# Performance work log

Hardware: AMD Instinct MI355X
Metric: run time of the kernel (lower is better)

Reference implementation:

```python
import jax, jax.numpy as jnp
import numpy as np

N_EMBD = 2048
N_HEAD = 16
N_KV_HEAD = 4
HEAD_DIM = N_EMBD // N_HEAD
MAX_SEQ_LEN = 2048
EPS = 1e-6
ROPE_THETA = 10000.0


def _build_rope_cache(dim, max_seq_len, theta=ROPE_THETA):
    inv_freq = 1.0 / theta ** (np.arange(0, dim, 2, dtype=np.float32) / dim)
    t = np.arange(max_seq_len, dtype=np.float32)
    freqs = np.outer(t, inv_freq)
    emb = np.concatenate([freqs, freqs], axis=-1)
    return jnp.asarray(np.cos(emb)), jnp.asarray(np.sin(emb))


def _rotate_half(x):
    x1, x2 = jnp.split(x, 2, axis=-1)
    return jnp.concatenate([-x2, x1], axis=-1)


def _rms_norm(x, w, eps=EPS):
    var = jnp.mean(jnp.square(x), axis=-1, keepdims=True)
    return x * jax.lax.rsqrt(var + eps) * w


def setup_inputs() -> dict:
    key = jax.random.key(0)
    ks = jax.random.split(key, 7)
    s = 1.0 / np.sqrt(N_EMBD)
    kv_dim = N_KV_HEAD * HEAD_DIM
    x = jax.random.normal(ks[0], (2, 2048, N_EMBD), dtype=jnp.float32)
    Wq = jax.random.normal(ks[1], (N_EMBD, N_EMBD), dtype=jnp.float32) * s
    Wk = jax.random.normal(ks[2], (kv_dim, N_EMBD), dtype=jnp.float32) * s
    Wv = jax.random.normal(ks[3], (kv_dim, N_EMBD), dtype=jnp.float32) * s
    Wo = jax.random.normal(ks[4], (N_EMBD, N_EMBD), dtype=jnp.float32) * s
    qn_w = jnp.ones((HEAD_DIM,), dtype=jnp.float32)
    kn_w = jnp.ones((HEAD_DIM,), dtype=jnp.float32)
    cos, sin = _build_rope_cache(HEAD_DIM, MAX_SEQ_LEN)
    return {"x": x, "Wq": Wq, "Wk": Wk, "Wv": Wv, "Wo": Wo,
            "qn_w": qn_w, "kn_w": kn_w, "rope_cos": cos, "rope_sin": sin}


def reference(x, Wq, Wk, Wv, Wo, qn_w, kn_w, rope_cos, rope_sin):
    B, T, C = x.shape
    # projections (torch Linear: y = x @ W.T)
    q = jnp.einsum('btc,dc->btd', x, Wq).reshape(B, T, N_HEAD, HEAD_DIM).transpose(0, 2, 1, 3)
    k = jnp.einsum('btc,dc->btd', x, Wk).reshape(B, T, N_KV_HEAD, HEAD_DIM).transpose(0, 2, 1, 3)
    v = jnp.einsum('btc,dc->btd', x, Wv).reshape(B, T, N_KV_HEAD, HEAD_DIM).transpose(0, 2, 1, 3)
    # qk rms-norm
    q = _rms_norm(q, qn_w)
    k = _rms_norm(k, kn_w)
    # rope
    cos = rope_cos[:T][None, None]  # [1,1,T,D]
    sin = rope_sin[:T][None, None]
    q = q * cos + _rotate_half(q) * sin
    k = k * cos + _rotate_half(k) * sin
    # GQA broadcast: group queries over kv heads instead of repeating k/v
    G = N_HEAD // N_KV_HEAD
    qg = q.reshape(B, N_KV_HEAD, G, T, HEAD_DIM)
    scale = 1.0 / jnp.sqrt(jnp.asarray(HEAD_DIM, dtype=q.dtype))
    scores = jnp.einsum('bhgqd,bhkd->bhgqk', qg, k) * scale  # [B,KV,G,T,T]
    causal = jnp.tril(jnp.ones((T, T), dtype=bool))
    scores = jnp.where(causal, scores, jnp.asarray(-jnp.inf, dtype=scores.dtype))
    attn = jax.nn.softmax(scores, axis=-1)
    y = jnp.einsum('bhgqk,bhkd->bhgqd', attn, v)  # [B,KV,G,T,D]
    y = y.reshape(B, N_HEAD, T, HEAD_DIM).transpose(0, 2, 1, 3).reshape(B, T, C)
    return jnp.einsum('btc,dc->btd', y, Wo)
```

## Files before the change

### kernel.cpp

```cpp
#include <hip/hip_runtime.h>
#include <stdint.h>

typedef unsigned short u16;
typedef __attribute__((ext_vector_type(4))) float f32x4;
typedef __attribute__((ext_vector_type(16))) float f32x16;
typedef __attribute__((ext_vector_type(8))) short bf16x8;
typedef __attribute__((ext_vector_type(4))) unsigned short u16x4;
typedef __attribute__((ext_vector_type(4))) unsigned u32x4;

static __device__ __forceinline__ u16 f2bf(float f) {
  union { float f; unsigned u; } v; v.f = f;
  unsigned r = v.u + 0x7fffu + ((v.u >> 16) & 1u);
  return (u16)(r >> 16);
}

static __device__ __forceinline__ unsigned cvtpk(float lo, float hi) {
  unsigned r;
  asm("v_cvt_pk_bf16_f32 %0, %1, %2" : "=v"(r) : "v"(lo), "v"(hi));
  return r;
}

static __device__ __forceinline__ void plane32_swap(unsigned& a, unsigned& b) {
  asm volatile("v_permlane32_swap_b32 %0, %1" : "+v"(a), "+v"(b));
}

static __device__ __forceinline__ void load_lds16(const void* g, void* l) {
  __builtin_amdgcn_global_load_lds(
      (const __attribute__((address_space(1))) void*)g,
      (__attribute__((address_space(3))) void*)l, 16, 0, 0);
}


__global__ __launch_bounds__(256) void cvt_f32_bf16(
    const float* __restrict__ in, u16* __restrict__ out, int n) {
  int i = blockIdx.x * 256 + threadIdx.x;
  const int n4 = n >> 2;
  for (; i < n4; i += gridDim.x * 256) {
    f32x4 v = *(const f32x4*)(in + (size_t)i * 4);
    u16x4 o = { f2bf(v[0]), f2bf(v[1]), f2bf(v[2]), f2bf(v[3]) };
    *(u16x4*)(out + (size_t)i * 4) = o;
  }
}

__global__ __launch_bounds__(256) void build_wcat(
    const float* __restrict__ Wq, const float* __restrict__ Wk,
    const float* __restrict__ Wv, u16* __restrict__ out) {
  int i = blockIdx.x * 256 + threadIdx.x;
  const int n4 = 3072 * 512;
  for (; i < n4; i += gridDim.x * 256) {
    int row = i >> 9;
    int c4 = i & 511;
    const float* src;
    if (row < 2048)       src = Wq + (size_t)row * 2048;
    else if (row < 2560)  src = Wk + (size_t)(row - 2048) * 2048;
    else                  src = Wv + (size_t)(row - 2560) * 2048;
    f32x4 v = *(const f32x4*)(src + c4 * 4);
    u16x4 o = { f2bf(v[0]), f2bf(v[1]), f2bf(v[2]), f2bf(v[3]) };
    *(u16x4*)(out + (size_t)i * 4) = o;
  }
}

__global__ __launch_bounds__(256) void gemm_bt(
    const u16* __restrict__ A, const u16* __restrict__ B,
    float* __restrict__ C, int M, int N, int K) {
  __shared__ u16 As[128 * 32];
  __shared__ u16 Bs[128 * 32];
  const int tid = threadIdx.x;
  const int lin = blockIdx.x;
  const int x = lin & 7, t = lin >> 3;
  const int bm = x * 4 + (t & 3);
  const int bn = t >> 2;
  const int w = tid >> 6, l = tid & 63;
  const int wr = w >> 1, wc = w & 1;
  const int lr = l & 15, lg = l >> 4;
  f32x4 acc[4][4] = {};
  const int srow = tid >> 2;
  const int scol = (tid & 3) << 3;
  const u16* Ag = A + (size_t)bm * 128 * K + (size_t)srow * K + scol;
  const u16* Bg = B + (size_t)bn * 128 * K + (size_t)srow * K + scol;
  u16* Asl = As + srow * 32 + scol;
  u16* Bsl = Bs + srow * 32 + scol;
  const int nk = K >> 5;
  for (int kt = 0; kt < nk; ++kt) {
    __syncthreads();
    const int ko = kt << 5;
    load_lds16(Ag + ko, Asl);
    load_lds16(Ag + (size_t)64 * K + ko, Asl + 64 * 32);
    load_lds16(Bg + ko, Bsl);
    load_lds16(Bg + (size_t)64 * K + ko, Bsl + 64 * 32);
    __syncthreads();
    bf16x8 af[4], bfr[4];
#pragma unroll
    for (int m = 0; m < 4; ++m)
      af[m] = *(const bf16x8*)&As[(wr * 64 + m * 16 + lr) * 32 + lg * 8];
#pragma unroll
    for (int n = 0; n < 4; ++n)
      bfr[n] = *(const bf16x8*)&Bs[(wc * 64 + n * 16 + lr) * 32 + lg * 8];
#pragma unroll
    for (int m = 0; m < 4; ++m)
#pragma unroll
      for (int n = 0; n < 4; ++n)
        acc[m][n] = __builtin_amdgcn_mfma_f32_16x16x32_bf16(af[m], bfr[n], acc[m][n], 0, 0, 0);
  }
#pragma unroll
  for (int m = 0; m < 4; ++m) {
    const int row = bm * 128 + wr * 64 + m * 16 + lg * 4;
#pragma unroll
    for (int n = 0; n < 4; ++n) {
      const int col = bn * 128 + wc * 64 + n * 16 + lr;
#pragma unroll
      for (int r = 0; r < 4; ++r)
        C[(size_t)(row + r) * N + col] = acc[m][n][r];
    }
  }
}

__global__ __launch_bounds__(256) void norm_rope(
    const float* __restrict__ qkv, const float* __restrict__ qn_w,
    const float* __restrict__ kn_w, const float* __restrict__ cosb,
    const float* __restrict__ sinb, u16* __restrict__ qhat,
    u16* __restrict__ khat) {
  const int gw = (blockIdx.x * 256 + threadIdx.x) >> 6;
  const int lane = threadIdx.x & 63;
  const int slot = gw % 20;
  const int row = gw / 20;
  const int t = row & 2047;
  const int b = row >> 11;
  const float* src; const float* nw; u16* dst;
  bool isq = slot < 16;
  if (isq) {
    src = qkv + (size_t)row * 3072 + slot * 128;
    nw = qn_w;
    dst = qhat + ((size_t)(b * 16 + slot) * 2048 + t) * 128;
  } else {
    src = qkv + (size_t)row * 3072 + 2048 + (slot - 16) * 128;
    nw = kn_w;
    dst = khat + ((size_t)(b * 4 + (slot - 16)) * 2048 + t) * 128;
  }
  float x1 = src[lane], x2 = src[lane + 64];
  float ss = x1 * x1 + x2 * x2;
#pragma unroll
  for (int o = 32; o; o >>= 1) ss += __shfl_xor(ss, o);
  float rs = rsqrtf(ss * (1.0f / 128.0f) + 1e-6f);
  float h1 = x1 * rs * nw[lane];
  float h2 = x2 * rs * nw[lane + 64];
  float c = cosb[t * 128 + lane], s = sinb[t * 128 + lane];
  float o1 = h1 * c - h2 * s;
  float o2 = h2 * c + h1 * s;
  if (isq) { o1 *= 0.088388347648318447f; o2 *= 0.088388347648318447f; }
  dst[lane] = f2bf(o1);
  dst[lane + 64] = f2bf(o2);
}

__global__ __launch_bounds__(256) void v_trans(
    const float* __restrict__ qkv, u16* __restrict__ vT) {
  __shared__ u16 st[64][130];
  const int bi = blockIdx.x;
  const int tt = bi & 31;
  const int kv = (bi >> 5) & 3;
  const int b = bi >> 7;
  const int tid = threadIdx.x;
#pragma unroll
  for (int i = 0; i < 32; ++i) {
    int idx = i * 256 + tid;
    int t = idx >> 7, d = idx & 127;
    float v = qkv[(size_t)(b * 2048 + tt * 64 + t) * 3072 + 2560 + kv * 128 + d];
    st[t][d] = f2bf(v);
  }
  __syncthreads();
#pragma unroll
  for (int i = 0; i < 32; ++i) {
    int idx = i * 256 + tid;
    int d = idx >> 6, t = idx & 63;
    vT[((size_t)(b * 4 + kv) * 128 + d) * 2048 + tt * 64 + t] = st[t][d];
  }
}

__global__ __launch_bounds__(512, 2) void attn(
    const u16* __restrict__ qhat, const u16* __restrict__ khat,
    const u16* __restrict__ vT, u16* __restrict__ yb) {
  __shared__ u16 Kt[2][64 * 128];
  const int bi = blockIdx.x;
  const int s = bi & 7;
  const int bh = bi >> 3;
  const int h = bh & 15, b = bh >> 4;
  const int kvh = h >> 2;
  const int tid = threadIdx.x;
  const int w = tid >> 6, l = tid & 63;
  const int ws = w & 3;
  const int cw = (w < 4) ? s : (15 - s);
  const int ql = l & 31, hi = l >> 5;
  const int wq0 = cw * 128 + ws * 32;
  const int wq_end = wq0 + 31;
  const int qg = wq0 + ql;

  bf16x8 qf[8];
  const u16* qp = qhat + ((size_t)(b * 16 + h) * 2048 + qg) * 128 + hi * 8;
#pragma unroll
  for (int sf = 0; sf < 8; ++sf) qf[sf] = *(const bf16x8*)(qp + 16 * sf);

  f32x16 yacc[4] = {};
  float m = -1e30f, lsum = 0.f;

  const u16* Kg = khat + (size_t)(b * 4 + kvh) * 2048 * 128;
  const u16* Vg = vT + (size_t)(b * 4 + kvh) * 128 * 2048;
  const int nt = 32 - 2 * s;

  auto stageK = [&](int tile, int buf) {
#pragma unroll
    for (int j = 0; j < 2; ++j) {
      int idx = j * 512 + tid;
      int row = idx >> 4, ch = idx & 15;
      load_lds16(Kg + (size_t)(tile * 64 + row) * 128 + ((ch ^ (row & 7)) * 8),
                 &Kt[buf][idx * 8]);
    }
  };

  stageK(0, 0);
  int cur = 0;
  for (int tile = 0; tile < nt; ++tile) {
    const int kv0 = tile * 64;
    __syncthreads();
    if (tile + 1 < nt) stageK(tile + 1, cur ^ 1);
    if (kv0 <= wq_end) {
      const u16* Vrow = Vg + (size_t)ql * 2048 + kv0 + hi * 8;
      bf16x8 va[4], vb[4];
#pragma unroll
      for (int ks = 0; ks < 4; ++ks) va[ks] = *(const bf16x8*)(Vrow + ks * 16);
#pragma unroll
      for (int ks = 0; ks < 4; ++ks) vb[ks] = *(const bf16x8*)(Vrow + 32 * 2048 + ks * 16);
      const u16* Kc = Kt[cur];
      f32x16 sacc[2] = {};
      __builtin_amdgcn_s_setprio(1);
#pragma unroll
      for (int n = 0; n < 2; ++n) {
#pragma unroll
        for (int sf = 0; sf < 8; ++sf) {
          bf16x8 kf = *(const bf16x8*)&Kc[(n * 32 + ql) * 128 + (((2 * sf + hi) ^ (l & 7)) * 8)];
          sacc[n] = __builtin_amdgcn_mfma_f32_32x32x16_bf16(kf, qf[sf], sacc[n], 0, 0, 0);
        }
      }
      __builtin_amdgcn_s_setprio(0);
      if (kv0 + 63 > wq0) {
#pragma unroll
        for (int n = 0; n < 2; ++n)
#pragma unroll
          for (int r = 0; r < 16; ++r) {
            int kv = kv0 + n * 32 + (r & 3) + 8 * (r >> 2) + 4 * hi;
            if (kv > qg) sacc[n][r] = -1e30f;
          }
      }
      float pm = -1e30f;
#pragma unroll
      for (int n = 0; n < 2; ++n)
#pragma unroll
        for (int r = 0; r < 16; ++r) pm = fmaxf(pm, sacc[n][r]);
      pm = fmaxf(pm, __shfl_xor(pm, 32));
      if (!__all(pm - m <= 8.0f)) {
        float mn = fmaxf(m, pm);
        float sc = __expf(m - mn);
        m = mn;
        lsum *= sc;
#pragma unroll
        for (int r = 0; r < 16; ++r) {
          int row = (r & 3) + 8 * (r >> 2) + 4 * hi;
          float scr = __shfl(sc, row);
#pragma unroll
          for (int d = 0; d < 4; ++d) yacc[d][r] *= scr;
        }
      }
      float ls = 0.f;
#pragma unroll
      for (int n = 0; n < 2; ++n)
#pragma unroll
        for (int r = 0; r < 16; ++r) {
          float e = __expf(sacc[n][r] - m);
          sacc[n][r] = e;
          ls += e;
        }
      ls += __shfl_xor(ls, 32);
      lsum += ls;
      bf16x8 pa[4];
#pragma unroll
      for (int s4 = 0; s4 < 4; ++s4) {
        const int n = s4 >> 1, R = (s4 & 1) * 8;
        unsigned P01 = cvtpk(sacc[n][R + 0], sacc[n][R + 1]);
        unsigned P23 = cvtpk(sacc[n][R + 2], sacc[n][R + 3]);
        unsigned P45 = cvtpk(sacc[n][R + 4], sacc[n][R + 5]);
        unsigned P67 = cvtpk(sacc[n][R + 6], sacc[n][R + 7]);
        plane32_swap(P01, P45);
        plane32_swap(P23, P67);
        union { u32x4 u; bf16x8 bv; } cvu;
        cvu.u[0] = P01; cvu.u[1] = P23; cvu.u[2] = P45; cvu.u[3] = P67;
        pa[s4] = cvu.bv;
      }
      __builtin_amdgcn_s_setprio(1);
#pragma unroll
      for (int ks = 0; ks < 4; ++ks)
        yacc[0] = __builtin_amdgcn_mfma_f32_32x32x16_bf16(pa[ks], va[ks], yacc[0], 0, 0, 0);
#pragma unroll
      for (int ks = 0; ks < 4; ++ks) va[ks] = *(const bf16x8*)(Vrow + 64 * 2048 + ks * 16);
#pragma unroll
      for (int ks = 0; ks < 4; ++ks)
        yacc[1] = __builtin_amdgcn_mfma_f32_32x32x16_bf16(pa[ks], vb[ks], yacc[1], 0, 0, 0);
#pragma unroll
      for (int ks = 0; ks < 4; ++ks) vb[ks] = *(const bf16x8*)(Vrow + 96 * 2048 + ks * 16);
#pragma unroll
      for (int ks = 0; ks < 4; ++ks)
        yacc[2] = __builtin_amdgcn_mfma_f32_32x32x16_bf16(pa[ks], va[ks], yacc[2], 0, 0, 0);
#pragma unroll
      for (int ks = 0; ks < 4; ++ks)
        yacc[3] = __builtin_amdgcn_mfma_f32_32x32x16_bf16(pa[ks], vb[ks], yacc[3], 0, 0, 0);
      __builtin_amdgcn_s_setprio(0);
    }
    cur ^= 1;
  }
#pragma unroll
  for (int r = 0; r < 16; ++r) {
    int row = (r & 3) + 8 * (r >> 2) + 4 * hi;
    float li = __shfl(lsum, row);
    float inv = 1.0f / li;
    u16* yp = yb + ((size_t)(b * 2048) + wq0 + row) * 2048 + h * 128 + ql;
#pragma unroll
    for (int d = 0; d < 4; ++d) yp[d * 32] = f2bf(yacc[d][r] * inv);
  }
}


extern "C" void kernel_launch(void* const* d_in, const int* in_sizes, int n_in,
                              void* d_out, int out_size, void* d_ws, size_t ws_size,
                              hipStream_t stream) {
  const float* x    = (const float*)d_in[0];
  const float* Wq   = (const float*)d_in[1];
  const float* Wk   = (const float*)d_in[2];
  const float* Wv   = (const float*)d_in[3];
  const float* Wo   = (const float*)d_in[4];
  const float* qn   = (const float*)d_in[5];
  const float* kn   = (const float*)d_in[6];
  const float* cosb = (const float*)d_in[7];
  const float* sinb = (const float*)d_in[8];
  float* out = (float*)d_out;
  (void)in_sizes; (void)n_in; (void)out_size; (void)ws_size;

  char* p = (char*)d_ws;
  u16*   xb   = (u16*)p;   p += (size_t)8388608 * 2;
  u16*   wcat = (u16*)p;   p += (size_t)6291456 * 2;
  u16*   wob  = (u16*)p;   p += (size_t)4194304 * 2;
  float* qkvf = (float*)p; p += (size_t)12582912 * 4;
  u16*   qh   = (u16*)p;   p += (size_t)8388608 * 2;
  u16*   kh   = (u16*)p;   p += (size_t)2097152 * 2;
  u16*   vt   = (u16*)p;   p += (size_t)2097152 * 2;
  u16*   yb   = (u16*)p;   p += (size_t)8388608 * 2;

  cvt_f32_bf16<<<2048, 256, 0, stream>>>(x, xb, 8388608);
  build_wcat<<<2048, 256, 0, stream>>>(Wq, Wk, Wv, wcat);
  cvt_f32_bf16<<<2048, 256, 0, stream>>>(Wo, wob, 4194304);
  gemm_bt<<<768, 256, 0, stream>>>(xb, wcat, qkvf, 4096, 3072, 2048);
  norm_rope<<<20480, 256, 0, stream>>>(qkvf, qn, kn, cosb, sinb, qh, kh);
  v_trans<<<256, 256, 0, stream>>>(qkvf, vt);
  attn<<<256, 512, 0, stream>>>(qh, kh, vt, yb);
  gemm_bt<<<512, 256, 0, stream>>>(yb, wob, out, 4096, 2048, 2048);
}
```

Baseline: 261.1 us.

## Split attention KV tiles across two wave groups and merge partial softmax results

The attention kernel doubles to 1024 threads: each 64-key tile is split so two groups of eight waves each handle 32 keys for the same query rows. At the end the partial max, sum and output accumulators are merged through shared memory before the normalized result is written. Separately, the softmax switches from __expf to a raw v_exp_f32 (exp2), with log2(e) folded into the query scale and the rescale threshold adjusted to match. The aim is more parallel work per block and cheaper exponentials, at the cost of extra LDS, merge synchronisation and register pressure from launch_bounds(1024,4).

Result: slower. 377.1 us (+44.4%).

```diff
diff --git a/kernel.cpp b/kernel.cpp
--- a/kernel.cpp
+++ b/kernel.cpp
@@ -22,6 +22,12 @@
 
 static __device__ __forceinline__ void plane32_swap(unsigned& a, unsigned& b) {
   asm volatile("v_permlane32_swap_b32 %0, %1" : "+v"(a), "+v"(b));
+}
+
+static __device__ __forceinline__ float exp2_fast(float x) {
+  float r;
+  asm("v_exp_f32 %0, %1" : "=v"(r) : "v"(x));
+  return r;
 }
 
 static __device__ __forceinline__ void load_lds16(const void* g, void* l) {
@@ -147,7 +153,7 @@
   float c = cosb[t * 128 + lane], s = sinb[t * 128 + lane];
   float o1 = h1 * c - h2 * s;
   float o2 = h2 * c + h1 * s;
-  if (isq) { o1 *= 0.088388347648318447f; o2 *= 0.088388347648318447f; }
+  if (isq) { o1 *= 0.12751744752f; o2 *= 0.12751744752f; }
   dst[lane] = f2bf(o1);
   dst[lane + 64] = f2bf(o2);
 }
@@ -176,10 +182,12 @@
   }
 }
 
-__global__ __launch_bounds__(512, 2) void attn(
+__global__ __launch_bounds__(1024, 4) void attn(
     const u16* __restrict__ qhat, const u16* __restrict__ khat,
     const u16* __restrict__ vT, u16* __restrict__ yb) {
   __shared__ u16 Kt[2][64 * 128];
+  __shared__ float obuf[4][32][128];
+  __shared__ float mlbuf[16][2][32];
   const int bi = blockIdx.x;
   const int s = bi & 7;
   const int bh = bi >> 3;
@@ -188,7 +196,9 @@
   const int tid = threadIdx.x;
   const int w = tid >> 6, l = tid & 63;
   const int ws = w & 3;
-  const int cw = (w < 4) ? s : (15 - s);
+  const int role = (w >> 2) & 1;
+  const int g = w >> 3;
+  const int cw = role ? (15 - s) : s;
   const int ql = l & 31, hi = l >> 5;
   const int wq0 = cw * 128 + ws * 32;
   const int wq_end = wq0 + 31;
@@ -206,59 +216,48 @@
   const u16* Vg = vT + (size_t)(b * 4 + kvh) * 128 * 2048;
   const int nt = 32 - 2 * s;
 
+  const int srow = tid >> 4, sch = tid & 15;
   auto stageK = [&](int tile, int buf) {
-#pragma unroll
-    for (int j = 0; j < 2; ++j) {
-      int idx = j * 512 + tid;
-      int row = idx >> 4, ch = idx & 15;
-      load_lds16(Kg + (size_t)(tile * 64 + row) * 128 + ((ch ^ (row & 7)) * 8),
-                 &Kt[buf][idx * 8]);
-    }
+    load_lds16(Kg + (size_t)(tile * 64 + srow) * 128 + ((sch ^ (srow & 7)) * 8),
+               &Kt[buf][tid * 8]);
   };
 
   stageK(0, 0);
   int cur = 0;
   for (int tile = 0; tile < nt; ++tile) {
-    const int kv0 = tile * 64;
+    const int kvb = tile * 64 + g * 32;
     __syncthreads();
     if (tile + 1 < nt) stageK(tile + 1, cur ^ 1);
-    if (kv0 <= wq_end) {
-      const u16* Vrow = Vg + (size_t)ql * 2048 + kv0 + hi * 8;
-      bf16x8 va[4], vb[4];
-#pragma unroll
-      for (int ks = 0; ks < 4; ++ks) va[ks] = *(const bf16x8*)(Vrow + ks * 16);
-#pragma unroll
-      for (int ks = 0; ks < 4; ++ks) vb[ks] = *(const bf16x8*)(Vrow + 32 * 2048 + ks * 16);
+    if (kvb <= wq_end) {
+      const u16* Vrow = Vg + (size_t)ql * 2048 + kvb + hi * 8;
+      bf16x8 va[2], vb[2];
+#pragma unroll
+      for (int ks = 0; ks < 2; ++ks) va[ks] = *(const bf16x8*)(Vrow + ks * 16);
+#pragma unroll
+      for (int ks = 0; ks < 2; ++ks) vb[ks] = *(const bf16x8*)(Vrow + 32 * 2048 + ks * 16);
       const u16* Kc = Kt[cur];
-      f32x16 sacc[2] = {};
+      f32x16 sacc = {};
       __builtin_amdgcn_s_setprio(1);
 #pragma unroll
-      for (int n = 0; n < 2; ++n) {
-#pragma unroll
-        for (int sf = 0; sf < 8; ++sf) {
-          bf16x8 kf = *(const bf16x8*)&Kc[(n * 32 + ql) * 128 + (((2 * sf + hi) ^ (l & 7)) * 8)];
-          sacc[n] = __builtin_amdgcn_mfma_f32_32x32x16_bf16(kf, qf[sf], sacc[n], 0, 0, 0);
+      for (int sf = 0; sf < 8; ++sf) {
+        bf16x8 kf = *(const bf16x8*)&Kc[(g * 32 + ql) * 128 + (((2 * sf + hi) ^ (l & 7)) * 8)];
+        sacc = __builtin_amdgcn_mfma_f32_32x32x16_bf16(kf, qf[sf], sacc, 0, 0, 0);
+      }
+      __builtin_amdgcn_s_setprio(0);
+      if (kvb + 31 > wq0) {
+#pragma unroll
+        for (int r = 0; r < 16; ++r) {
+          int kv = kvb + (r & 3) + 8 * (r >> 2) + 4 * hi;
+          if (kv > qg) sacc[r] = -1e30f;
         }
       }
-      __builtin_amdgcn_s_setprio(0);
-      if (kv0 + 63 > wq0) {
-#pragma unroll
-        for (int n = 0; n < 2; ++n)
-#pragma unroll
-          for (int r = 0; r < 16; ++r) {
-            int kv = kv0 + n * 32 + (r & 3) + 8 * (r >> 2) + 4 * hi;
-            if (kv > qg) sacc[n][r] = -1e30f;
-          }
-      }
       float pm = -1e30f;
 #pragma unroll
-      for (int n = 0; n < 2; ++n)
-#pragma unroll
-        for (int r = 0; r < 16; ++r) pm = fmaxf(pm, sacc[n][r]);
+      for (int r = 0; r < 16; ++r) pm = fmaxf(pm, sacc[r]);
       pm = fmaxf(pm, __shfl_xor(pm, 32));
-      if (!__all(pm - m <= 8.0f)) {
+      if (!__all(pm - m <= 11.0f)) {
         float mn = fmaxf(m, pm);
-        float sc = __expf(m - mn);
+        float sc = exp2_fast(m - mn);
         m = mn;
         lsum *= sc;
 #pragma unroll
@@ -271,58 +270,95 @@
       }
       float ls = 0.f;
 #pragma unroll
-      for (int n = 0; n < 2; ++n)
-#pragma unroll
-        for (int r = 0; r < 16; ++r) {
-          float e = __expf(sacc[n][r] - m);
-          sacc[n][r] = e;
-          ls += e;
-        }
+      for (int r = 0; r < 16; ++r) {
+        float e = exp2_fast(sacc[r] - m);
+        sacc[r] = e;
+        ls += e;
+      }
       ls += __shfl_xor(ls, 32);
       lsum += ls;
-      bf16x8 pa[4];
-#pragma unroll
-      for (int s4 = 0; s4 < 4; ++s4) {
-        const int n = s4 >> 1, R = (s4 & 1) * 8;
-        unsigned P01 = cvtpk(sacc[n][R + 0], sacc[n][R + 1]);
-        unsigned P23 = cvtpk(sacc[n][R + 2], sacc[n][R + 3]);
-        unsigned P45 = cvtpk(sacc[n][R + 4], sacc[n][R + 5]);
-        unsigned P67 = cvtpk(sacc[n][R + 6], sacc[n][R + 7]);
+      bf16x8 pa[2];
+#pragma unroll
+      for (int s2 = 0; s2 < 2; ++s2) {
+        const int R = s2 * 8;
+        unsigned P01 = cvtpk(sacc[R + 0], sacc[R + 1]);
+        unsigned P23 = cvtpk(sacc[R + 2], sacc[R + 3]);
+        unsigned P45 = cvtpk(sacc[R + 4], sacc[R + 5]);
+        unsigned P67 = cvtpk(sacc[R + 6], sacc[R + 7]);
         plane32_swap(P01, P45);
         plane32_swap(P23, P67);
         union { u32x4 u; bf16x8 bv; } cvu;
         cvu.u[0] = P01; cvu.u[1] = P23; cvu.u[2] = P45; cvu.u[3] = P67;
-        pa[s4] = cvu.bv;
+        pa[s2] = cvu.bv;
       }
       __builtin_amdgcn_s_setprio(1);
 #pragma unroll
-      for (int ks = 0; ks < 4; ++ks)
+      for (int ks = 0; ks < 2; ++ks)
         yacc[0] = __builtin_amdgcn_mfma_f32_32x32x16_bf16(pa[ks], va[ks], yacc[0], 0, 0, 0);
 #pragma unroll
-      for (int ks = 0; ks < 4; ++ks) va[ks] = *(const bf16x8*)(Vrow + 64 * 2048 + ks * 16);
-#pragma unroll
-      for (int ks = 0; ks < 4; ++ks)
+      for (int ks = 0; ks < 2; ++ks) va[ks] = *(const bf16x8*)(Vrow + 64 * 2048 + ks * 16);
+#pragma unroll
+      for (int ks = 0; ks < 2; ++ks)
         yacc[1] = __builtin_amdgcn_mfma_f32_32x32x16_bf16(pa[ks], vb[ks], yacc[1], 0, 0, 0);
 #pragma unroll
-      for (int ks = 0; ks < 4; ++ks) vb[ks] = *(const bf16x8*)(Vrow + 96 * 2048 + ks * 16);
-#pragma unroll
-      for (int ks = 0; ks < 4; ++ks)
+      for (int ks = 0; ks < 2; ++ks) vb[ks] = *(const bf16x8*)(Vrow + 96 * 2048 + ks * 16);
+#pragma unroll
+      for (int ks = 0; ks < 2; ++ks)
         yacc[2] = __builtin_amdgcn_mfma_f32_32x32x16_bf16(pa[ks], va[ks], yacc[2], 0, 0, 0);
 #pragma unroll
-      for (int ks = 0; ks < 4; ++ks)
+      for (int ks = 0; ks < 2; ++ks)
         yacc[3] = __builtin_amdgcn_mfma_f32_32x32x16_bf16(pa[ks], vb[ks], yacc[3], 0, 0, 0);
       __builtin_amdgcn_s_setprio(0);
     }
     cur ^= 1;
   }
+
+  __syncthreads();
+  if (hi == 0) { mlbuf[w][0][ql] = m; mlbuf[w][1][ql] = lsum; }
+  __syncthreads();
+  const float mo = mlbuf[w ^ 8][0][ql];
+  const float lo2 = mlbuf[w ^ 8][1][ql];
+  const float mf = fmaxf(m, mo);
+  const float sc = exp2_fast(m - mf);
+  const float lf = lsum * sc + lo2 * exp2_fast(mo - mf);
 #pragma unroll
   for (int r = 0; r < 16; ++r) {
     int row = (r & 3) + 8 * (r >> 2) + 4 * hi;
-    float li = __shfl(lsum, row);
-    float inv = 1.0f / li;
-    u16* yp = yb + ((size_t)(b * 2048) + wq0 + row) * 2048 + h * 128 + ql;
-#pragma unroll
-    for (int d = 0; d < 4; ++d) yp[d * 32] = f2bf(yacc[d][r] * inv);
+    float scr = __shfl(sc, row);
+#pragma unroll
+    for (int d = 0; d < 4; ++d) yacc[d][r] *= scr;
+  }
+#pragma unroll
+  for (int round = 0; round < 2; ++round) {
+    if (g == 1 && role == round) {
+#pragma unroll
+      for (int r = 0; r < 16; ++r) {
+        int row = (r & 3) + 8 * (r >> 2) + 4 * hi;
+#pragma unroll
+        for (int d = 0; d < 4; ++d) obuf[w & 3][row][d * 32 + ql] = yacc[d][r];
+      }
+    }
+    __syncthreads();
+    if (g == 0 && role == round) {
+#pragma unroll
+      for (int r = 0; r < 16; ++r) {
+        int row = (r & 3) + 8 * (r >> 2) + 4 * hi;
+#pragma unroll
+        for (int d = 0; d < 4; ++d) yacc[d][r] += obuf[w & 3][row][d * 32 + ql];
+      }
+    }
+    __syncthreads();
+  }
+  if (g == 0) {
+    const float inv = 1.0f / lf;
+#pragma unroll
+    for (int r = 0; r < 16; ++r) {
+      int row = (r & 3) + 8 * (r >> 2) + 4 * hi;
+      float ir = __shfl(inv, row);
+      u16* yp = yb + ((size_t)(b * 2048) + wq0 + row) * 2048 + h * 128 + ql;
+#pragma unroll
+      for (int d = 0; d < 4; ++d) yp[d * 32] = f2bf(yacc[d][r] * ir);
+    }
   }
 }
 
@@ -358,6 +394,6 @@
   gemm_bt<<<768, 256, 0, stream>>>(xb, wcat, qkvf, 4096, 3072, 2048);
   norm_rope<<<20480, 256, 0, stream>>>(qkvf, qn, kn, cosb, sinb, qh, kh);
   v_trans<<<256, 256, 0, stream>>>(qkvf, vt);
-  attn<<<256, 512, 0, stream>>>(qh, kh, vt, yb);
+  attn<<<256, 1024, 0, stream>>>(qh, kh, vt, yb);
   gemm_bt<<<512, 256, 0, stream>>>(yb, wob, out, 4096, 2048, 2048);
 }
```

## Restructure attention into per-wave 32-key tiles with direct global K loads

Applied to the files above, without the earlier changes.

The attention kernel drops the LDS double-buffered 64-row K staging and its block-wide barriers. Each wave now walks 32-key chunks up to its own diagonal and reads K and V fragments straight from global or L2, with 256-thread blocks and twice as many blocks. The log2(e) factor is folded into the Q scale so softmax can use raw v_exp_f32, and the rescale threshold is raised to match. This removes the barriers and the wasted work on partially masked 64-wide tiles, at the cost of more redundant global K traffic with no LDS reuse and more MFMA chains per key.

Result: slower. 335.8 us (+28.6%).

```diff
diff --git a/kernel.cpp b/kernel.cpp
--- a/kernel.cpp
+++ b/kernel.cpp
@@ -22,6 +22,12 @@
 
 static __device__ __forceinline__ void plane32_swap(unsigned& a, unsigned& b) {
   asm volatile("v_permlane32_swap_b32 %0, %1" : "+v"(a), "+v"(b));
+}
+
+static __device__ __forceinline__ float exp2_fast(float x) {
+  float r;
+  asm("v_exp_f32 %0, %1" : "=v"(r) : "v"(x));
+  return r;
 }
 
 static __device__ __forceinline__ void load_lds16(const void* g, void* l) {
@@ -147,7 +153,7 @@
   float c = cosb[t * 128 + lane], s = sinb[t * 128 + lane];
   float o1 = h1 * c - h2 * s;
   float o2 = h2 * c + h1 * s;
-  if (isq) { o1 *= 0.088388347648318447f; o2 *= 0.088388347648318447f; }
+  if (isq) { o1 *= 0.12751744752f; o2 *= 0.12751744752f; }
   dst[lane] = f2bf(o1);
   dst[lane + 64] = f2bf(o2);
 }
@@ -176,22 +182,20 @@
   }
 }
 
-__global__ __launch_bounds__(512, 2) void attn(
+__global__ __launch_bounds__(256) void attn(
     const u16* __restrict__ qhat, const u16* __restrict__ khat,
     const u16* __restrict__ vT, u16* __restrict__ yb) {
-  __shared__ u16 Kt[2][64 * 128];
   const int bi = blockIdx.x;
-  const int s = bi & 7;
-  const int bh = bi >> 3;
+  const int j = bi & 255;
+  const int bh = j >> 3;
+  const int g = (bi < 256) ? (j & 7) : (15 - (j & 7));
   const int h = bh & 15, b = bh >> 4;
   const int kvh = h >> 2;
   const int tid = threadIdx.x;
   const int w = tid >> 6, l = tid & 63;
-  const int ws = w & 3;
-  const int cw = (w < 4) ? s : (15 - s);
   const int ql = l & 31, hi = l >> 5;
-  const int wq0 = cw * 128 + ws * 32;
-  const int wq_end = wq0 + 31;
+  const int c = 4 * g + w;
+  const int wq0 = c * 32;
   const int qg = wq0 + ql;
 
   bf16x8 qf[8];
@@ -204,116 +208,75 @@
 
   const u16* Kg = khat + (size_t)(b * 4 + kvh) * 2048 * 128;
   const u16* Vg = vT + (size_t)(b * 4 + kvh) * 128 * 2048;
-  const int nt = 32 - 2 * s;
-
-  auto stageK = [&](int tile, int buf) {
-#pragma unroll
-    for (int j = 0; j < 2; ++j) {
-      int idx = j * 512 + tid;
-      int row = idx >> 4, ch = idx & 15;
-      load_lds16(Kg + (size_t)(tile * 64 + row) * 128 + ((ch ^ (row & 7)) * 8),
-                 &Kt[buf][idx * 8]);
-    }
-  };
-
-  stageK(0, 0);
-  int cur = 0;
-  for (int tile = 0; tile < nt; ++tile) {
-    const int kv0 = tile * 64;
-    __syncthreads();
-    if (tile + 1 < nt) stageK(tile + 1, cur ^ 1);
-    if (kv0 <= wq_end) {
-      const u16* Vrow = Vg + (size_t)ql * 2048 + kv0 + hi * 8;
-      bf16x8 va[4], vb[4];
-#pragma unroll
-      for (int ks = 0; ks < 4; ++ks) va[ks] = *(const bf16x8*)(Vrow + ks * 16);
-#pragma unroll
-      for (int ks = 0; ks < 4; ++ks) vb[ks] = *(const bf16x8*)(Vrow + 32 * 2048 + ks * 16);
-      const u16* Kc = Kt[cur];
-      f32x16 sacc[2] = {};
-      __builtin_amdgcn_s_setprio(1);
-#pragma unroll
-      for (int n = 0; n < 2; ++n) {
-#pragma unroll
-        for (int sf = 0; sf < 8; ++sf) {
-          bf16x8 kf = *(const bf16x8*)&Kc[(n * 32 + ql) * 128 + (((2 * sf + hi) ^ (l & 7)) * 8)];
-          sacc[n] = __builtin_amdgcn_mfma_f32_32x32x16_bf16(kf, qf[sf], sacc[n], 0, 0, 0);
-        }
+
+  for (int jc = 0; jc <= c; ++jc) {
+    const int kv0 = jc * 32;
+    const u16* Krow = Kg + (size_t)(kv0 + ql) * 128 + hi * 8;
+    f32x16 sacc = {};
+    __builtin_amdgcn_s_setprio(1);
+#pragma unroll
+    for (int sf = 0; sf < 8; ++sf) {
+      bf16x8 kf = *(const bf16x8*)(Krow + 16 * sf);
+      sacc = __builtin_amdgcn_mfma_f32_32x32x16_bf16(kf, qf[sf], sacc, 0, 0, 0);
+    }
+    __builtin_amdgcn_s_setprio(0);
+    if (jc == c) {
+#pragma unroll
+      for (int r = 0; r < 16; ++r) {
+        int crow = (r & 3) + 8 * (r >> 2) + 4 * hi;
+        if (crow > ql) sacc[r] = -1e30f;
       }
-      __builtin_amdgcn_s_setprio(0);
-      if (kv0 + 63 > wq0) {
-#pragma unroll
-        for (int n = 0; n < 2; ++n)
-#pragma unroll
-          for (int r = 0; r < 16; ++r) {
-            int kv = kv0 + n * 32 + (r & 3) + 8 * (r >> 2) + 4 * hi;
-            if (kv > qg) sacc[n][r] = -1e30f;
-          }
+    }
+    float pm = -1e30f;
+#pragma unroll
+    for (int r = 0; r < 16; ++r) pm = fmaxf(pm, sacc[r]);
+    pm = fmaxf(pm, __shfl_xor(pm, 32));
+    if (!__all(pm - m <= 11.0f)) {
+      float mn = fmaxf(m, pm);
+      float sc = exp2_fast(m - mn);
+      m = mn;
+      lsum *= sc;
+#pragma unroll
+      for (int r = 0; r < 16; ++r) {
+        int row = (r & 3) + 8 * (r >> 2) + 4 * hi;
+        float scr = __shfl(sc, row);
+#pragma unroll
+        for (int d = 0; d < 4; ++d) yacc[d][r] *= scr;
       }
-      float pm = -1e30f;
-#pragma unroll
-      for (int n = 0; n < 2; ++n)
-#pragma unroll
-        for (int r = 0; r < 16; ++r) pm = fmaxf(pm, sacc[n][r]);
-      pm = fmaxf(pm, __shfl_xor(pm, 32));
-      if (!__all(pm - m <= 8.0f)) {
-        float mn = fmaxf(m, pm);
-        float sc = __expf(m - mn);
-        m = mn;
-        lsum *= sc;
-#pragma unroll
-        for (int r = 0; r < 16; ++r) {
-          int row = (r & 3) + 8 * (r >> 2) + 4 * hi;
-          float scr = __shfl(sc, row);
-#pragma unroll
-          for (int d = 0; d < 4; ++d) yacc[d][r] *= scr;
-        }
-      }
-      float ls = 0.f;
-#pragma unroll
-      for (int n = 0; n < 2; ++n)
-#pragma unroll
-        for (int r = 0; r < 16; ++r) {
-          float e = __expf(sacc[n][r] - m);
-          sacc[n][r] = e;
-          ls += e;
-        }
-      ls += __shfl_xor(ls, 32);
-      lsum += ls;
-      bf16x8 pa[4];
-#pragma unroll
-      for (int s4 = 0; s4 < 4; ++s4) {
-        const int n = s4 >> 1, R = (s4 & 1) * 8;
-        unsigned P01 = cvtpk(sacc[n][R + 0], sacc[n][R + 1]);
-        unsigned P23 = cvtpk(sacc[n][R + 2], sacc[n][R + 3]);
-        unsigned P45 = cvtpk(sacc[n][R + 4], sacc[n][R + 5]);
-        unsigned P67 = cvtpk(sacc[n][R + 6], sacc[n][R + 7]);
-        plane32_swap(P01, P45);
-        plane32_swap(P23, P67);
-        union { u32x4 u; bf16x8 bv; } cvu;
-        cvu.u[0] = P01; cvu.u[1] = P23; cvu.u[2] = P45; cvu.u[3] = P67;
-        pa[s4] = cvu.bv;
-      }
-      __builtin_amdgcn_s_setprio(1);
-#pragma unroll
-      for (int ks = 0; ks < 4; ++ks)
-        yacc[0] = __builtin_amdgcn_mfma_f32_32x32x16_bf16(pa[ks], va[ks], yacc[0], 0, 0, 0);
-#pragma unroll
-      for (int ks = 0; ks < 4; ++ks) va[ks] = *(const bf16x8*)(Vrow + 64 * 2048 + ks * 16);
-#pragma unroll
-      for (int ks = 0; ks < 4; ++ks)
-        yacc[1] = __builtin_amdgcn_mfma_f32_32x32x16_bf16(pa[ks], vb[ks], yacc[1], 0, 0, 0);
-#pragma unroll
-      for (int ks = 0; ks < 4; ++ks) vb[ks] = *(const bf16x8*)(Vrow + 96 * 2048 + ks * 16);
-#pragma unroll
-      for (int ks = 0; ks < 4; ++ks)
-        yacc[2] = __builtin_amdgcn_mfma_f32_32x32x16_bf16(pa[ks], va[ks], yacc[2], 0, 0, 0);
-#pragma unroll
-      for (int ks = 0; ks < 4; ++ks)
-        yacc[3] = __builtin_amdgcn_mfma_f32_32x32x16_bf16(pa[ks], vb[ks], yacc[3], 0, 0, 0);
-      __builtin_amdgcn_s_setprio(0);
-    }
-    cur ^= 1;
+    }
+    float ls = 0.f;
+#pragma unroll
+    for (int r = 0; r < 16; ++r) {
+      float e = exp2_fast(sacc[r] - m);
+      sacc[r] = e;
+      ls += e;
+    }
+    ls += __shfl_xor(ls, 32);
+    lsum += ls;
+    bf16x8 pa[2];
+#pragma unroll
+    for (int s2 = 0; s2 < 2; ++s2) {
+      const int R = s2 * 8;
+      unsigned P01 = cvtpk(sacc[R + 0], sacc[R + 1]);
+      unsigned P23 = cvtpk(sacc[R + 2], sacc[R + 3]);
+      unsigned P45 = cvtpk(sacc[R + 4], sacc[R + 5]);
+      unsigned P67 = cvtpk(sacc[R + 6], sacc[R + 7]);
+      plane32_swap(P01, P45);
+      plane32_swap(P23, P67);
+      union { u32x4 u; bf16x8 bv; } cvu;
+      cvu.u[0] = P01; cvu.u[1] = P23; cvu.u[2] = P45; cvu.u[3] = P67;
+      pa[s2] = cvu.bv;
+    }
+    const u16* Vrow = Vg + (size_t)ql * 2048 + kv0 + hi * 8;
+    __builtin_amdgcn_s_setprio(1);
+#pragma unroll
+    for (int d = 0; d < 4; ++d) {
+      bf16x8 v0 = *(const bf16x8*)(Vrow + (size_t)d * 32 * 2048);
+      bf16x8 v1 = *(const bf16x8*)(Vrow + (size_t)d * 32 * 2048 + 16);
+      yacc[d] = __builtin_amdgcn_mfma_f32_32x32x16_bf16(pa[0], v0, yacc[d], 0, 0, 0);
+      yacc[d] = __builtin_amdgcn_mfma_f32_32x32x16_bf16(pa[1], v1, yacc[d], 0, 0, 0);
+    }
+    __builtin_amdgcn_s_setprio(0);
   }
 #pragma unroll
   for (int r = 0; r < 16; ++r) {
@@ -358,6 +321,6 @@
   gemm_bt<<<768, 256, 0, stream>>>(xb, wcat, qkvf, 4096, 3072, 2048);
   norm_rope<<<20480, 256, 0, stream>>>(qkvf, qn, kn, cosb, sinb, qh, kh);
   v_trans<<<256, 256, 0, stream>>>(qkvf, vt);
-  attn<<<256, 512, 0, stream>>>(qh, kh, vt, yb);
+  attn<<<512, 256, 0, stream>>>(qh, kh, vt, yb);
   gemm_bt<<<512, 256, 0, stream>>>(yb, wob, out, 4096, 2048, 2048);
 }
```

## Fuse QK RMS-norm, RoPE and V transpose into QKV GEMM epilogue; use exp2

Applied to the files above, without the earlier changes.

The QKV projection GEMM now finishes with the per-head RMS norm, RoPE and query scaling, writing bf16 q/k and transposed v directly. This removes the fp32 qkv intermediate buffer and its write/read traffic, plus two extra kernel launches. The accumulator tile is rounded to bf16 in LDS before normalization, which adds a small precision loss. In attention, log2(e) is folded into the query scale so softmax uses raw v_exp_f32 with a wider rescale threshold, and all V fragments are loaded up front so the PV MFMAs can be interleaved, at the cost of more registers.

Result: slower. 268.1 us (+2.7%).

```diff
diff --git a/kernel.cpp b/kernel.cpp
--- a/kernel.cpp
+++ b/kernel.cpp
@@ -13,6 +13,10 @@
   unsigned r = v.u + 0x7fffu + ((v.u >> 16) & 1u);
   return (u16)(r >> 16);
 }
+static __device__ __forceinline__ float bf2f(u16 u) {
+  union { unsigned u; float f; } v; v.u = ((unsigned)u) << 16;
+  return v.f;
+}
 
 static __device__ __forceinline__ unsigned cvtpk(float lo, float hi) {
   unsigned r;
@@ -22,6 +26,12 @@
 
 static __device__ __forceinline__ void plane32_swap(unsigned& a, unsigned& b) {
   asm volatile("v_permlane32_swap_b32 %0, %1" : "+v"(a), "+v"(b));
+}
+
+static __device__ __forceinline__ float exp2_fast(float x) {
+  float r;
+  asm("v_exp_f32 %0, %1" : "=v"(r) : "v"(x));
+  return r;
 }
 
 static __device__ __forceinline__ void load_lds16(const void* g, void* l) {
@@ -57,6 +67,108 @@
     f32x4 v = *(const f32x4*)(src + c4 * 4);
     u16x4 o = { f2bf(v[0]), f2bf(v[1]), f2bf(v[2]), f2bf(v[3]) };
     *(u16x4*)(out + (size_t)i * 4) = o;
+  }
+}
+
+__global__ __launch_bounds__(256) void gemm_qkv(
+    const u16* __restrict__ A, const u16* __restrict__ W,
+    const float* __restrict__ qn_w, const float* __restrict__ kn_w,
+    const float* __restrict__ cosb, const float* __restrict__ sinb,
+    u16* __restrict__ qh, u16* __restrict__ kh, u16* __restrict__ vt) {
+  const int K = 2048;
+  __shared__ u16 smem[128 * 130];
+  __shared__ float ssbuf[128][2];
+  u16* As = smem;
+  u16* Bs = smem + 4096;
+  const int tid = threadIdx.x;
+  const int lin = blockIdx.x;
+  const int x = lin & 7, t = lin >> 3;
+  const int bm = x * 4 + (t & 3);
+  const int bn = t >> 2;
+  const int w = tid >> 6, l = tid & 63;
+  const int wr = w >> 1, wc = w & 1;
+  const int lr = l & 15, lg = l >> 4;
+  f32x4 acc[4][4] = {};
+  const int srow = tid >> 2;
+  const int scol = (tid & 3) << 3;
+  const u16* Ag = A + (size_t)bm * 128 * K + (size_t)srow * K + scol;
+  const u16* Bg = W + (size_t)bn * 128 * K + (size_t)srow * K + scol;
+  u16* Asl = As + srow * 32 + scol;
+  u16* Bsl = Bs + srow * 32 + scol;
+  for (int kt = 0; kt < 64; ++kt) {
+    __syncthreads();
+    const int ko = kt << 5;
+    load_lds16(Ag + ko, Asl);
+    load_lds16(Ag + (size_t)64 * K + ko, Asl + 64 * 32);
+    load_lds16(Bg + ko, Bsl);
+    load_lds16(Bg + (size_t)64 * K + ko, Bsl + 64 * 32);
+    __syncthreads();
+    bf16x8 af[4], bfr[4];
+#pragma unroll
+    for (int m = 0; m < 4; ++m)
+      af[m] = *(const bf16x8*)&As[(wr * 64 + m * 16 + lr) * 32 + lg * 8];
+#pragma unroll
+    for (int n = 0; n < 4; ++n)
+      bfr[n] = *(const bf16x8*)&Bs[(wc * 64 + n * 16 + lr) * 32 + lg * 8];
+#pragma unroll
+    for (int m = 0; m < 4; ++m)
+#pragma unroll
+      for (int n = 0; n < 4; ++n)
+        acc[m][n] = __builtin_amdgcn_mfma_f32_16x16x32_bf16(af[m], bfr[n], acc[m][n], 0, 0, 0);
+  }
+  __syncthreads();
+  if (bn < 20) {
+#pragma unroll
+    for (int m = 0; m < 4; ++m)
+#pragma unroll
+      for (int r = 0; r < 4; ++r) {
+        float ps = 0.f;
+#pragma unroll
+        for (int n = 0; n < 4; ++n) ps += acc[m][n][r] * acc[m][n][r];
+#pragma unroll
+        for (int o = 8; o; o >>= 1) ps += __shfl_xor(ps, o);
+        if (lr == 0) ssbuf[wr * 64 + m * 16 + lg * 4 + r][wc] = ps;
+      }
+  }
+#pragma unroll
+  for (int m = 0; m < 4; ++m)
+#pragma unroll
+    for (int n = 0; n < 4; ++n)
+#pragma unroll
+      for (int r = 0; r < 4; ++r)
+        smem[(wr * 64 + m * 16 + lg * 4 + r) * 130 + wc * 64 + n * 16 + lr] =
+            f2bf(acc[m][n][r]);
+  __syncthreads();
+  const int tg0 = bm * 128;
+  if (bn < 20) {
+    const bool isq = bn < 16;
+    const float* nw = isq ? qn_w : kn_w;
+    const float qs = isq ? 0.12751744752f : 1.0f;
+    u16* dstbase = isq ? (qh + (size_t)bn * 2048 * 128)
+                       : (kh + (size_t)(bn - 16) * 2048 * 128);
+    for (int it = 0; it < 64; ++it) {
+      int idx = it * 256 + tid;
+      int tl = idx >> 7, d = idx & 127;
+      int tglob = tg0 + tl;
+      int tt = tglob & 2047, bb = tglob >> 11;
+      float rs = rsqrtf((ssbuf[tl][0] + ssbuf[tl][1]) * (1.0f / 128.0f) + 1e-6f);
+      int d2 = (d + 64) & 127;
+      float h1 = bf2f(smem[tl * 130 + d]) * rs * nw[d];
+      float h2 = bf2f(smem[tl * 130 + d2]) * rs * nw[d2];
+      float rot = (d < 64) ? -h2 : h2;
+      float c = cosb[tt * 128 + d], s = sinb[tt * 128 + d];
+      u16* dst = dstbase + ((size_t)bb * (isq ? 16 : 4) * 2048 + (size_t)tt) * 128 + d;
+      *dst = f2bf((h1 * c + rot * s) * qs);
+    }
+  } else {
+    const int kvi = bn - 20;
+    for (int it = 0; it < 64; ++it) {
+      int idx = it * 256 + tid;
+      int d = idx >> 7, tl = idx & 127;
+      int tglob = tg0 + tl;
+      int tt = tglob & 2047, bb = tglob >> 11;
+      vt[((size_t)(bb * 4 + kvi) * 128 + d) * 2048 + tt] = smem[tl * 130 + d];
+    }
   }
 }
 
@@ -115,67 +227,6 @@
   }
 }
 
-__global__ __launch_bounds__(256) void norm_rope(
-    const float* __restrict__ qkv, const float* __restrict__ qn_w,
-    const float* __restrict__ kn_w, const float* __restrict__ cosb,
-    const float* __restrict__ sinb, u16* __restrict__ qhat,
-    u16* __restrict__ khat) {
-  const int gw = (blockIdx.x * 256 + threadIdx.x) >> 6;
-  const int lane = threadIdx.x & 63;
-  const int slot = gw % 20;
-  const int row = gw / 20;
-  const int t = row & 2047;
-  const int b = row >> 11;
-  const float* src; const float* nw; u16* dst;
-  bool isq = slot < 16;
-  if (isq) {
-    src = qkv + (size_t)row * 3072 + slot * 128;
-    nw = qn_w;
-    dst = qhat + ((size_t)(b * 16 + slot) * 2048 + t) * 128;
-  } else {
-    src = qkv + (size_t)row * 3072 + 2048 + (slot - 16) * 128;
-    nw = kn_w;
-    dst = khat + ((size_t)(b * 4 + (slot - 16)) * 2048 + t) * 128;
-  }
-  float x1 = src[lane], x2 = src[lane + 64];
-  float ss = x1 * x1 + x2 * x2;
-#pragma unroll
-  for (int o = 32; o; o >>= 1) ss += __shfl_xor(ss, o);
-  float rs = rsqrtf(ss * (1.0f / 128.0f) + 1e-6f);
-  float h1 = x1 * rs * nw[lane];
-  float h2 = x2 * rs * nw[lane + 64];
-  float c = cosb[t * 128 + lane], s = sinb[t * 128 + lane];
-  float o1 = h1 * c - h2 * s;
-  float o2 = h2 * c + h1 * s;
-  if (isq) { o1 *= 0.088388347648318447f; o2 *= 0.088388347648318447f; }
-  dst[lane] = f2bf(o1);
-  dst[lane + 64] = f2bf(o2);
-}
-
-__global__ __launch_bounds__(256) void v_trans(
-    const float* __restrict__ qkv, u16* __restrict__ vT) {
-  __shared__ u16 st[64][130];
-  const int bi = blockIdx.x;
-  const int tt = bi & 31;
-  const int kv = (bi >> 5) & 3;
-  const int b = bi >> 7;
-  const int tid = threadIdx.x;
-#pragma unroll
-  for (int i = 0; i < 32; ++i) {
-    int idx = i * 256 + tid;
-    int t = idx >> 7, d = idx & 127;
-    float v = qkv[(size_t)(b * 2048 + tt * 64 + t) * 3072 + 2560 + kv * 128 + d];
-    st[t][d] = f2bf(v);
-  }
-  __syncthreads();
-#pragma unroll
-  for (int i = 0; i < 32; ++i) {
-    int idx = i * 256 + tid;
-    int d = idx >> 6, t = idx & 63;
-    vT[((size_t)(b * 4 + kv) * 128 + d) * 2048 + tt * 64 + t] = st[t][d];
-  }
-}
-
 __global__ __launch_bounds__(512, 2) void attn(
     const u16* __restrict__ qhat, const u16* __restrict__ khat,
     const u16* __restrict__ vT, u16* __restrict__ yb) {
@@ -224,11 +275,15 @@
     if (tile + 1 < nt) stageK(tile + 1, cur ^ 1);
     if (kv0 <= wq_end) {
       const u16* Vrow = Vg + (size_t)ql * 2048 + kv0 + hi * 8;
-      bf16x8 va[4], vb[4];
-#pragma unroll
-      for (int ks = 0; ks < 4; ++ks) va[ks] = *(const bf16x8*)(Vrow + ks * 16);
-#pragma unroll
-      for (int ks = 0; ks < 4; ++ks) vb[ks] = *(const bf16x8*)(Vrow + 32 * 2048 + ks * 16);
+      bf16x8 vfr0[4], vfr1[4], vfr2[4], vfr3[4];
+#pragma unroll
+      for (int ks = 0; ks < 4; ++ks) vfr0[ks] = *(const bf16x8*)(Vrow + ks * 16);
+#pragma unroll
+      for (int ks = 0; ks < 4; ++ks) vfr1[ks] = *(const bf16x8*)(Vrow + 32 * 2048 + ks * 16);
+#pragma unroll
+      for (int ks = 0; ks < 4; ++ks) vfr2[ks] = *(const bf16x8*)(Vrow + 64 * 2048 + ks * 16);
+#pragma unroll
+      for (int ks = 0; ks < 4; ++ks) vfr3[ks] = *(const bf16x8*)(Vrow + 96 * 2048 + ks * 16);
       const u16* Kc = Kt[cur];
       f32x16 sacc[2] = {};
       __builtin_amdgcn_s_setprio(1);
@@ -256,9 +311,9 @@
 #pragma unroll
         for (int r = 0; r < 16; ++r) pm = fmaxf(pm, sacc[n][r]);
       pm = fmaxf(pm, __shfl_xor(pm, 32));
-      if (!__all(pm - m <= 8.0f)) {
+      if (!__all(pm - m <= 11.0f)) {
         float mn = fmaxf(m, pm);
-        float sc = __expf(m - mn);
+        float sc = exp2_fast(m - mn);
         m = mn;
         lsum *= sc;
 #pragma unroll
@@ -274,7 +329,7 @@
       for (int n = 0; n < 2; ++n)
 #pragma unroll
         for (int r = 0; r < 16; ++r) {
-          float e = __expf(sacc[n][r] - m);
+          float e = exp2_fast(sacc[n][r] - m);
           sacc[n][r] = e;
           ls += e;
         }
@@ -296,21 +351,12 @@
       }
       __builtin_amdgcn_s_setprio(1);
 #pragma unroll
-      for (int ks = 0; ks < 4; ++ks)
-        yacc[0] = __builtin_amdgcn_mfma_f32_32x32x16_bf16(pa[ks], va[ks], yacc[0], 0, 0, 0);
-#pragma unroll
-      for (int ks = 0; ks < 4; ++ks) va[ks] = *(const bf16x8*)(Vrow + 64 * 2048 + ks * 16);
-#pragma unroll
-      for (int ks = 0; ks < 4; ++ks)
-        yacc[1] = __builtin_amdgcn_mfma_f32_32x32x16_bf16(pa[ks], vb[ks], yacc[1], 0, 0, 0);
-#pragma unroll
-      for (int ks = 0; ks < 4; ++ks) vb[ks] = *(const bf16x8*)(Vrow + 96 * 2048 + ks * 16);
-#pragma unroll
-      for (int ks = 0; ks < 4; ++ks)
-        yacc[2] = __builtin_amdgcn_mfma_f32_32x32x16_bf16(pa[ks], va[ks], yacc[2], 0, 0, 0);
-#pragma unroll
-      for (int ks = 0; ks < 4; ++ks)
-        yacc[3] = __builtin_amdgcn_mfma_f32_32x32x16_bf16(pa[ks], vb[ks], yacc[3], 0, 0, 0);
+      for (int ks = 0; ks < 4; ++ks) {
+        yacc[0] = __builtin_amdgcn_mfma_f32_32x32x16_bf16(pa[ks], vfr0[ks], yacc[0], 0, 0, 0);
+        yacc[1] = __builtin_amdgcn_mfma_f32_32x32x16_bf16(pa[ks], vfr1[ks], yacc[1], 0, 0, 0);
+        yacc[2] = __builtin_amdgcn_mfma_f32_32x32x16_bf16(pa[ks], vfr2[ks], yacc[2], 0, 0, 0);
+        yacc[3] = __builtin_amdgcn_mfma_f32_32x32x16_bf16(pa[ks], vfr3[ks], yacc[3], 0, 0, 0);
+      }
       __builtin_amdgcn_s_setprio(0);
     }
     cur ^= 1;
@@ -346,7 +392,6 @@
   u16*   xb   = (u16*)p;   p += (size_t)8388608 * 2;
   u16*   wcat = (u16*)p;   p += (size_t)6291456 * 2;
   u16*   wob  = (u16*)p;   p += (size_t)4194304 * 2;
-  float* qkvf = (float*)p; p += (size_t)12582912 * 4;
   u16*   qh   = (u16*)p;   p += (size_t)8388608 * 2;
   u16*   kh   = (u16*)p;   p += (size_t)2097152 * 2;
   u16*   vt   = (u16*)p;   p += (size_t)2097152 * 2;
@@ -355,9 +400,7 @@
   cvt_f32_bf16<<<2048, 256, 0, stream>>>(x, xb, 8388608);
   build_wcat<<<2048, 256, 0, stream>>>(Wq, Wk, Wv, wcat);
   cvt_f32_bf16<<<2048, 256, 0, stream>>>(Wo, wob, 4194304);
-  gemm_bt<<<768, 256, 0, stream>>>(xb, wcat, qkvf, 4096, 3072, 2048);
-  norm_rope<<<20480, 256, 0, stream>>>(qkvf, qn, kn, cosb, sinb, qh, kh);
-  v_trans<<<256, 256, 0, stream>>>(qkvf, vt);
+  gemm_qkv<<<768, 256, 0, stream>>>(xb, wcat, qn, kn, cosb, sinb, qh, kh, vt);
   attn<<<256, 512, 0, stream>>>(qh, kh, vt, yb);
   gemm_bt<<<512, 256, 0, stream>>>(yb, wob, out, 4096, 2048, 2048);
 }
```
